# Optimization experiments

Measured on AMD Instinct MI355X. Metric: run time of the kernel, lower is better.

Reference implementation:

```python
import jax, jax.numpy as jnp
import numpy as np

N, E, D, R, G, C = 100000, 600000, 128, 4, 256, 16
EPS = 1e-5

def _rgcn(x, src, dst, edge_type, w_rel, w_root, b):
    # out_i = x_i @ W_root + b + sum_r mean_{j in N_r(i)} x_j @ W_r  (PyG RGCNConv, aggr='mean')
    x_src = x[src]                                   # [E, D] gather
    out = x @ w_root + b                             # [N, D]
    for r in range(R):
        m = (edge_type == r).astype(x.dtype)         # [E]
        msg = (x_src @ w_rel[r]) * m[:, None]        # [E, D]
        agg = jax.ops.segment_sum(msg, dst, num_segments=N)
        cnt = jax.ops.segment_sum(m, dst, num_segments=N)
        out = out + agg / jnp.maximum(cnt, 1.0)[:, None]
    return out

def _bn_eval(x, gamma, beta, mean, var):
    return (x - mean) * jax.lax.rsqrt(var + EPS) * gamma + beta

def setup_inputs() -> dict:
    key = jax.random.key(0)
    ks = jax.random.split(key, 12)
    x = jax.random.normal(ks[0], (N, D), dtype=jnp.float32)
    edge_index = jax.random.randint(ks[1], (2, E), 0, N)
    edge_type = jax.random.randint(ks[2], (E,), 0, R)
    batch = jnp.sort(jax.random.randint(ks[3], (N,), 0, G))
    s = 1.0 / np.sqrt(D)
    conv_rel_w = jax.random.normal(ks[4], (3, R, D, D), dtype=jnp.float32) * s
    conv_root_w = jax.random.normal(ks[5], (3, D, D), dtype=jnp.float32) * s
    conv_bias = jnp.zeros((3, D), dtype=jnp.float32)
    bn_gamma = jnp.ones((2, D), dtype=jnp.float32)
    bn_beta = jnp.zeros((2, D), dtype=jnp.float32)
    bn_mean = jax.random.normal(ks[6], (2, D), dtype=jnp.float32) * 0.1
    bn_var = jax.random.uniform(ks[7], (2, D), minval=0.5, maxval=1.5, dtype=jnp.float32)
    cls_w1 = jax.random.normal(ks[8], (D, D // 2), dtype=jnp.float32) * s
    cls_b1 = jnp.zeros((D // 2,), dtype=jnp.float32)
    cls_w2 = jax.random.normal(ks[9], (D // 2, C), dtype=jnp.float32) / np.sqrt(D // 2)
    cls_b2 = jnp.zeros((C,), dtype=jnp.float32)
    return {"x": x, "edge_index": edge_index, "edge_type": edge_type, "batch": batch,
            "conv_rel_w": conv_rel_w, "conv_root_w": conv_root_w, "conv_bias": conv_bias,
            "bn_gamma": bn_gamma, "bn_beta": bn_beta, "bn_mean": bn_mean, "bn_var": bn_var,
            "cls_w1": cls_w1, "cls_b1": cls_b1, "cls_w2": cls_w2, "cls_b2": cls_b2}

def reference(x, edge_index, edge_type, batch, conv_rel_w, conv_root_w, conv_bias,
              bn_gamma, bn_beta, bn_mean, bn_var, cls_w1, cls_b1, cls_w2, cls_b2):
    src, dst = edge_index[0], edge_index[1]
    prev = None
    h = x
    for i in range(3):
        h_new = _rgcn(h, src, dst, edge_type, conv_rel_w[i], conv_root_w[i], conv_bias[i])
        if prev is not None:
            h_new = h_new + prev  # residual (shapes always match: D==D)
        if i != 2:
            h_new = _bn_eval(h_new, bn_gamma[i], bn_beta[i], bn_mean[i], bn_var[i])
            h_new = jax.nn.elu(h_new)  # alpha=1; dropout inactive in eval
        prev = h_new
        h = h_new
    # global mean pool over graphs
    sums = jax.ops.segment_sum(h, batch, num_segments=G)          # [G, D]
    cnts = jax.ops.segment_sum(jnp.ones((N,), h.dtype), batch, num_segments=G)
    pooled = sums / jnp.maximum(cnts, 1.0)[:, None]
    z = jax.nn.elu(pooled @ cls_w1 + cls_b1)
    logits = z @ cls_w2 + cls_b2
    return jax.nn.log_softmax(logits, axis=-1)
```

## Files before the change

kernel.cpp:

```cpp
#include <hip/hip_runtime.h>
#include <hip/hip_bf16.h>

#define NN 100000
#define EE 600000
#define DD 128
#define GG 256
#define CCL 16

typedef __attribute__((ext_vector_type(8))) short short8;
typedef __attribute__((ext_vector_type(4))) float f32x4;
typedef const __attribute__((address_space(1))) void* gas_t;
typedef __attribute__((address_space(3))) void* las_t;

__device__ __forceinline__ void async_ld16(const void* g, void* l) {
    __builtin_amdgcn_global_load_lds((gas_t)g, (las_t)l, 16, 0, 0);
}
__device__ __forceinline__ unsigned short f2bf(float x) {
    unsigned u = __float_as_uint(x);
    unsigned r = (u + 0x7FFFu + ((u >> 16) & 1u)) >> 16;
    return (unsigned short)r;
}
__device__ __forceinline__ float bf2f(unsigned short b) {
    return __uint_as_float(((unsigned)b) << 16);
}
__device__ __forceinline__ void unpack8(uint4 v, float* f) {
    f[0] = __uint_as_float(v.x << 16); f[1] = __uint_as_float(v.x & 0xFFFF0000u);
    f[2] = __uint_as_float(v.y << 16); f[3] = __uint_as_float(v.y & 0xFFFF0000u);
    f[4] = __uint_as_float(v.z << 16); f[5] = __uint_as_float(v.z & 0xFFFF0000u);
    f[6] = __uint_as_float(v.w << 16); f[7] = __uint_as_float(v.w & 0xFFFF0000u);
}

__global__ __launch_bounds__(256) void sniff_kernel(const void* __restrict__ xraw, int* __restrict__ flag) {
    int t = threadIdx.x;
    const unsigned short* u = (const unsigned short*)xraw;
    int good = 0;
    #pragma unroll
    for (int i = 0; i < 4; i++) {
        unsigned short b = u[t * 4 + i];
        int e = (b >> 7) & 0xFF;
        if (e >= 107 && e <= 130) good++;
    }
    __shared__ int sg[256];
    sg[t] = good;
    __syncthreads();
    for (int s = 128; s > 0; s >>= 1) { if (t < s) sg[t] += sg[t + s]; __syncthreads(); }
    if (t == 0) flag[0] = (sg[0] >= 900) ? 1 : 0;
}

__device__ __forceinline__ float loadf(const void* p, size_t i, int isbf) {
    if (isbf) return bf2f(((const unsigned short*)p)[i]);
    return ((const float*)p)[i];
}

__global__ __launch_bounds__(256) void convx_kernel(const void* __restrict__ xraw, const int* __restrict__ flag,
                                                    __hip_bfloat16* __restrict__ xc) {
    int isbf = flag[0];
    size_t i0 = ((size_t)blockIdx.x * 256 + threadIdx.x) * 8;
    if (i0 >= (size_t)NN * DD) return;
    if (isbf) {
        *(uint4*)(xc + i0) = *(const uint4*)((const __hip_bfloat16*)xraw + i0);
    } else {
        const float* xf = (const float*)xraw;
        unsigned short o[8];
        #pragma unroll
        for (int j = 0; j < 8; j++) o[j] = f2bf(xf[i0 + j]);
        *(uint4*)(xc + i0) = *(uint4*)o;
    }
}

__global__ __launch_bounds__(256) void convw_kernel(const void* __restrict__ rel_raw, const void* __restrict__ root_raw,
                                                    const int* __restrict__ flag, __hip_bfloat16* __restrict__ wt) {
    int isbf = flag[0];
    int mat = blockIdx.x;
    int layer = mat / 5, g = mat % 5;
    size_t srcoff = (g == 0) ? (size_t)layer * 16384 : (size_t)(layer * 4 + (g - 1)) * 16384;
    const void* sraw = (g == 0) ? root_raw : rel_raw;
    __hip_bfloat16* dstp = wt + (size_t)mat * 16384;
    for (int idx = threadIdx.x; idx < 16384; idx += 256) {
        int k = idx >> 7, n = idx & 127;
        float v = loadf(sraw, srcoff + (size_t)k * 128 + n, isbf);
        dstp[n * 128 + k] = __float2bfloat16(v);
    }
}

__global__ __launch_bounds__(256) void convp_kernel(const void* bias, const void* bng, const void* bnb,
                                                    const void* bnm, const void* bnv, const void* w1,
                                                    const void* b1, const void* w2, const void* b2,
                                                    const int* __restrict__ flag, float* __restrict__ pf) {
    int isbf = flag[0];
    int b = blockIdx.x, t = threadIdx.x;
    if (b < 9) {
        const void* srcs[9] = {bias, bng, bnb, bnm, bnv, w1, b1, w2, b2};
        const int cnts[9] = {384, 256, 256, 256, 256, 8192, 64, 1024, 16};
        const int offs[9] = {0, 384, 640, 896, 1152, 1408, 9600, 9664, 10688};
        const void* s = srcs[b];
        int c = cnts[b], o = offs[b];
        for (int i = t; i < c; i += 256) pf[o + i] = loadf(s, i, isbf);
    } else {
        int bl = b - 9;
        if (t < 128) {
            float iva = rsqrtf(loadf(bnv, bl * 128 + t, isbf) + 1e-5f);
            float gm = loadf(bng, bl * 128 + t, isbf) * iva;
            float ga = loadf(bnb, bl * 128 + t, isbf) - loadf(bnm, bl * 128 + t, isbf) * gm;
            pf[11008 + bl * 256 + t] = gm;
            pf[11008 + bl * 256 + 128 + t] = ga;
        }
    }
}

__global__ __launch_bounds__(256) void count4_kernel(const int* __restrict__ dst, const int* __restrict__ et,
                                                     int* __restrict__ cnt4) {
    int e = blockIdx.x * 256 + threadIdx.x;
    if (e < EE) atomicAdd(&cnt4[dst[e] * 4 + et[e]], 1);
}

__global__ __launch_bounds__(256) void allocn_kernel(const int* __restrict__ cnt4, int* __restrict__ counter,
                                                     int* __restrict__ startn, int* __restrict__ wptr4) {
    int n = blockIdx.x * 256 + threadIdx.x;
    int lane = threadIdx.x & 63;
    int4 cv = make_int4(0, 0, 0, 0);
    int c = 0;
    if (n < NN) {
        cv = *(const int4*)(cnt4 + n * 4);
        c = cv.x + cv.y + cv.z + cv.w;
    }
    int v = c;
    #pragma unroll
    for (int d = 1; d < 64; d <<= 1) {
        int o = __shfl_up(v, d);
        if (lane >= d) v += o;
    }
    int base = 0;
    if (lane == 63) base = atomicAdd(counter, v);
    base = __shfl(base, 63);
    if (n < NN) {
        int s = base + v - c;
        startn[n] = s;
        wptr4[n * 4 + 0] = s;
        wptr4[n * 4 + 1] = s + cv.x;
        wptr4[n * 4 + 2] = s + cv.x + cv.y;
        wptr4[n * 4 + 3] = s + cv.x + cv.y + cv.z;
    }
}

__global__ __launch_bounds__(256) void fill4_kernel(const int* __restrict__ src, const int* __restrict__ dst,
                                                    const int* __restrict__ et, int* __restrict__ wptr4,
                                                    int* __restrict__ esrc) {
    int e = blockIdx.x * 256 + threadIdx.x;
    if (e < EE) {
        int pos = atomicAdd(&wptr4[dst[e] * 4 + et[e]], 1);
        esrc[pos] = src[e];
    }
}

__global__ __launch_bounds__(256) void agg_kernel(const __hip_bfloat16* __restrict__ h,
                                                  const int* __restrict__ esrc,
                                                  const int* __restrict__ startn,
                                                  const int* __restrict__ cnt4,
                                                  __hip_bfloat16* __restrict__ Abuf) {
    int node = blockIdx.x * 16 + (threadIdx.x >> 4);
    int c16 = threadIdx.x & 15;
    int col0 = c16 * 8;
    int4 cv = *(const int4*)(cnt4 + node * 4);
    int s = startn[node];
    int cr[4] = {cv.x, cv.y, cv.z, cv.w};
    #pragma unroll
    for (int r = 0; r < 4; r++) {
        int c = cr[r];
        float a[8];
        #pragma unroll
        for (int j = 0; j < 8; j++) a[j] = 0.f;
        int i = 0;
        for (; i + 4 <= c; i += 4) {
            int s4[4];
            uint4 vv[4];
            #pragma unroll
            for (int q = 0; q < 4; q++) s4[q] = esrc[s + i + q];
            #pragma unroll
            for (int q = 0; q < 4; q++) vv[q] = *(const uint4*)(h + (size_t)s4[q] * 128 + col0);
            #pragma unroll
            for (int q = 0; q < 4; q++) {
                float f[8];
                unpack8(vv[q], f);
                #pragma unroll
                for (int j = 0; j < 8; j++) a[j] += f[j];
            }
        }
        for (; i < c; i++) {
            int sq = esrc[s + i];
            uint4 v0 = *(const uint4*)(h + (size_t)sq * 128 + col0);
            float f[8];
            unpack8(v0, f);
            #pragma unroll
            for (int j = 0; j < 8; j++) a[j] += f[j];
        }
        float w = (c > 0) ? (1.f / (float)c) : 0.f;
        unsigned short u[8];
        #pragma unroll
        for (int j = 0; j < 8; j++) u[j] = f2bf(a[j] * w);
        *(uint4*)(Abuf + (size_t)node * 512 + r * 128 + col0) = *(uint4*)u;
        s += c;
    }
}

#define STAGE_B(P, CH) do { \
    const __hip_bfloat16* _wg = wt5 + (size_t)(CH) * 16384; \
    _Pragma("unroll") \
    for (int _j = 0; _j < 4; _j++) { \
        int _slot = _j * 512 + t; \
        int _brow = _slot >> 4, _sp = _slot & 15; \
        async_ld16(_wg + _brow * 128 + (_sp ^ (_brow & 15)) * 8, &ldsb[(P) * 16384 + _slot * 8]); \
    } \
} while (0)

#define LOAD_A(D0, D1, CH) do { \
    const __hip_bfloat16* _p0 = ((CH) == 0) ? (h_in + (size_t)r0 * 128) : (Abuf + (size_t)r0 * 512 + ((CH) - 1) * 128); \
    const __hip_bfloat16* _p1 = ((CH) == 0) ? (h_in + (size_t)r1 * 128) : (Abuf + (size_t)r1 * 512 + ((CH) - 1) * 128); \
    _Pragma("unroll") \
    for (int _kc = 0; _kc < 4; _kc++) { \
        D0[_kc] = *(const short8*)(_p0 + _kc * 32 + quad * 8); \
        D1[_kc] = *(const short8*)(_p1 + _kc * 32 + quad * 8); \
    } \
} while (0)

#define MFMA_CH(P, A0, A1) do { \
    _Pragma("unroll") \
    for (int _kc = 0; _kc < 4; _kc++) { \
        int _s = _kc * 4 + quad; \
        _Pragma("unroll") \
        for (int _nt = 0; _nt < 4; _nt++) { \
            int _rb = wc * 64 + _nt * 16 + r16; \
            short8 _b = *(const short8*)&ldsb[(P) * 16384 + (_rb * 16 + (_s ^ (_rb & 15))) * 8]; \
            acc0[_nt] = __builtin_amdgcn_mfma_f32_16x16x32_bf16(A0[_kc], _b, acc0[_nt], 0, 0, 0); \
            acc1[_nt] = __builtin_amdgcn_mfma_f32_16x16x32_bf16(A1[_kc], _b, acc1[_nt], 0, 0, 0); \
        } \
    } \
} while (0)

__global__ __launch_bounds__(512, 4) void rgemm_kernel(const __hip_bfloat16* __restrict__ h_in,
                                                       const __hip_bfloat16* __restrict__ Abuf,
                                                       const __hip_bfloat16* __restrict__ wt5,
                                                       const float* __restrict__ bias,
                                                       const float* __restrict__ gmp,
                                                       const float* __restrict__ gap,
                                                       const __hip_bfloat16* __restrict__ hres,
                                                       __hip_bfloat16* __restrict__ hout,
                                                       int do_bn) {
    __shared__ __align__(16) char ldsraw[132 * 128 * 4];
    short* ldsb = (short*)ldsraw;
    float* cf = (float*)ldsraw;
    int t = threadIdx.x;
    int wave = t >> 6, lane = t & 63, quad = lane >> 4, r16 = lane & 15;
    int wr = wave & 3, wc = wave >> 2;
    int m0 = blockIdx.x * 128;

    int r0 = m0 + wr * 32 + r16;      if (r0 > NN - 1) r0 = NN - 1;
    int r1 = m0 + wr * 32 + 16 + r16; if (r1 > NN - 1) r1 = NN - 1;

    f32x4 acc0[4], acc1[4];
    #pragma unroll
    for (int j = 0; j < 4; j++) { acc0[j] = (f32x4){0.f, 0.f, 0.f, 0.f}; acc1[j] = (f32x4){0.f, 0.f, 0.f, 0.f}; }

    short8 aA0[4], aA1[4], aB0[4], aB1[4];
    LOAD_A(aA0, aA1, 0);
    STAGE_B(0, 0);

    __syncthreads();  STAGE_B(1, 1);  LOAD_A(aB0, aB1, 1);  MFMA_CH(0, aA0, aA1);
    __syncthreads();  STAGE_B(0, 2);  LOAD_A(aA0, aA1, 2);  MFMA_CH(1, aB0, aB1);
    __syncthreads();  STAGE_B(1, 3);  LOAD_A(aB0, aB1, 3);  MFMA_CH(0, aA0, aA1);
    __syncthreads();  STAGE_B(0, 4);  LOAD_A(aA0, aA1, 4);  MFMA_CH(1, aB0, aB1);
    __syncthreads();                                        MFMA_CH(0, aA0, aA1);

    __syncthreads();
    #pragma unroll
    for (int nt = 0; nt < 4; nt++) {
        int col = wc * 64 + nt * 16 + r16;
        #pragma unroll
        for (int reg = 0; reg < 4; reg++) {
            int crow0 = wr * 32 + quad * 4 + reg;
            cf[crow0 * 132 + col] = acc0[nt][reg];
            cf[(crow0 + 16) * 132 + col] = acc1[nt][reg];
        }
    }
    __syncthreads();
    #pragma unroll
    for (int it = 0; it < 4; it++) {
        int u4 = it * 512 + t;
        int crow = u4 >> 4, seg = u4 & 15;
        int node = m0 + crow;
        if (node < NN) {
            int gcol0 = seg * 8;
            float a[8];
            #pragma unroll
            for (int j = 0; j < 8; j++) a[j] = cf[crow * 132 + gcol0 + j] + bias[gcol0 + j];
            if (hres) {
                float rf[8];
                unpack8(*(const uint4*)(hres + (size_t)node * 128 + gcol0), rf);
                #pragma unroll
                for (int j = 0; j < 8; j++) a[j] += rf[j];
            }
            if (do_bn) {
                #pragma unroll
                for (int j = 0; j < 8; j++) {
                    float z = a[j] * gmp[gcol0 + j] + gap[gcol0 + j];
                    a[j] = z > 0.f ? z : expm1f(z);
                }
            }
            unsigned short u[8];
            #pragma unroll
            for (int j = 0; j < 8; j++) u[j] = f2bf(a[j]);
            *(uint4*)(hout + (size_t)node * 128 + gcol0) = *(uint4*)u;
        }
    }
}

__global__ __launch_bounds__(256) void pool_kernel(const __hip_bfloat16* __restrict__ h3,
                                                   const int* __restrict__ batch,
                                                   float* __restrict__ pooled) {
    int g = blockIdx.x, t = threadIdx.x;
    int rowpar = t >> 4, colg = t & 15;
    int lo = 0, hi = NN;
    while (lo < hi) { int mid = (lo + hi) >> 1; if (batch[mid] < g) lo = mid + 1; else hi = mid; }
    int s0 = lo;
    hi = NN;
    while (lo < hi) { int mid = (lo + hi) >> 1; if (batch[mid] < g + 1) lo = mid + 1; else hi = mid; }
    int s1 = lo;
    float a[8];
    #pragma unroll
    for (int j = 0; j < 8; j++) a[j] = 0.f;
    for (int n = s0 + rowpar; n < s1; n += 16) {
        float f[8];
        unpack8(*(const uint4*)(h3 + (size_t)n * 128 + colg * 8), f);
        #pragma unroll
        for (int j = 0; j < 8; j++) a[j] += f[j];
    }
    __shared__ float sd[16][128];
    #pragma unroll
    for (int j = 0; j < 8; j++) sd[rowpar][colg * 8 + j] = a[j];
    __syncthreads();
    if (t < 128) {
        float sum = 0.f;
        #pragma unroll
        for (int i = 0; i < 16; i++) sum += sd[i][t];
        int cgn = s1 - s0;
        pooled[g * 128 + t] = sum / (float)(cgn > 0 ? cgn : 1);
    }
}

__global__ __launch_bounds__(64) void cls_kernel(const float* __restrict__ pooled,
                                                 const float* __restrict__ pf,
                                                 const int* __restrict__ flag,
                                                 void* __restrict__ out) {
    int g = blockIdx.x, j = threadIdx.x;
    const float* w1 = pf + 1408;
    const float* b1 = pf + 9600;
    const float* w2 = pf + 9664;
    const float* b2 = pf + 10688;
    __shared__ float z[64];
    __shared__ float lg[16];
    const float* p = pooled + g * 128;
    float acc = b1[j];
    for (int d = 0; d < 128; d++) acc += p[d] * w1[d * 64 + j];
    acc = acc > 0.f ? acc : expm1f(acc);
    z[j] = acc;
    __syncthreads();
    if (j < CCL) {
        float l = b2[j];
        for (int k = 0; k < 64; k++) l += z[k] * w2[k * 16 + j];
        lg[j] = l;
    }
    __syncthreads();
    if (j < CCL) {
        float m = lg[0];
        for (int k = 1; k < CCL; k++) m = fmaxf(m, lg[k]);
        float s = 0.f;
        for (int k = 0; k < CCL; k++) s += expf(lg[k] - m);
        float val = lg[j] - m - logf(s);
        if (flag[0]) ((__hip_bfloat16*)out)[g * CCL + j] = __float2bfloat16(val);
        else         ((float*)out)[g * CCL + j] = val;
    }
}

extern "C" void kernel_launch(void* const* d_in, const int* in_sizes, int n_in,
                              void* d_out, int out_size, void* d_ws, size_t ws_size,
                              hipStream_t stream) {
    const void* x_raw    = d_in[0];
    const int* ei        = (const int*)d_in[1];
    const int* et        = (const int*)d_in[2];
    const int* batch     = (const int*)d_in[3];
    const void* rel_raw  = d_in[4];
    const void* root_raw = d_in[5];
    const int* srcp = ei;
    const int* dstp = ei + EE;

    char* ws = (char*)d_ws;
    size_t off = 0;
    auto take = [&](size_t bytes) { size_t r = off; off += (bytes + 1023) & ~(size_t)1023; return r; };
    __hip_bfloat16* Abuf  = (__hip_bfloat16*)(ws + take((size_t)NN * 512 * 2));
    __hip_bfloat16* xc    = (__hip_bfloat16*)(ws + take((size_t)NN * 128 * 2));
    __hip_bfloat16* hA    = (__hip_bfloat16*)(ws + take((size_t)NN * 128 * 2));
    __hip_bfloat16* hB    = (__hip_bfloat16*)(ws + take((size_t)NN * 128 * 2));
    __hip_bfloat16* hC    = (__hip_bfloat16*)(ws + take((size_t)NN * 128 * 2));
    __hip_bfloat16* wt    = (__hip_bfloat16*)(ws + take((size_t)15 * 16384 * 2));
    float* pf             = (float*)(ws + take((size_t)11520 * 4));
    float* pooled         = (float*)(ws + take((size_t)GG * 128 * 4));
    int* cnt4             = (int*)(ws + take((size_t)NN * 16 + 8));
    int* counter          = cnt4 + NN * 4;
    int* flag             = cnt4 + NN * 4 + 1;
    int* startn           = (int*)(ws + take((size_t)NN * 4));
    int* wptr4            = (int*)(ws + take((size_t)NN * 16));
    int* esrc             = (int*)(ws + take((size_t)EE * 4));

    hipMemsetAsync(cnt4, 0, (size_t)NN * 16 + 4, stream);
    sniff_kernel<<<1, 256, 0, stream>>>(x_raw, flag);
    convx_kernel<<<(NN * DD / 8 + 255) / 256, 256, 0, stream>>>(x_raw, flag, xc);
    convw_kernel<<<15, 256, 0, stream>>>(rel_raw, root_raw, flag, wt);
    convp_kernel<<<11, 256, 0, stream>>>(d_in[6], d_in[7], d_in[8], d_in[9], d_in[10],
                                         d_in[11], d_in[12], d_in[13], d_in[14], flag, pf);
    count4_kernel<<<(EE + 255) / 256, 256, 0, stream>>>(dstp, et, cnt4);
    allocn_kernel<<<(NN + 255) / 256, 256, 0, stream>>>(cnt4, counter, startn, wptr4);
    fill4_kernel<<<(EE + 255) / 256, 256, 0, stream>>>(srcp, dstp, et, wptr4, esrc);

    const __hip_bfloat16* hin = xc;
    __hip_bfloat16* houts[3] = {hA, hB, hC};
    for (int l = 0; l < 3; l++) {
        int bl = l < 2 ? l : 1;
        agg_kernel<<<NN / 16, 256, 0, stream>>>(hin, esrc, startn, cnt4, Abuf);
        rgemm_kernel<<<(NN + 127) / 128, 512, 0, stream>>>(
            hin, Abuf, wt + (size_t)l * 5 * 16384, pf + l * 128,
            pf + 11008 + bl * 256, pf + 11008 + bl * 256 + 128,
            (l > 0) ? hin : (const __hip_bfloat16*)nullptr, houts[l], (l < 2) ? 1 : 0);
        hin = houts[l];
    }
    pool_kernel<<<GG, 256, 0, stream>>>(houts[2], batch, pooled);
    cls_kernel<<<GG, 64, 0, stream>>>(pooled, pf, flag, (void*)d_out);
}
```

Measured before the change: 651.9 us.

## Fuse neighbor aggregation into the relational GEMM kernel, dropping the Abuf round trip

Replaces the separate aggregation kernel and LDS-staged GEMM with one per-layer kernel. Each lane gathers and averages its node's neighbor rows per relation straight into MFMA A-fragments, then multiplies against weights read directly from global memory. This removes the 100000x512 bf16 intermediate buffer's write and read plus one launch per layer. In exchange, weight B-fragments are no longer shared through LDS and are re-read per wave from cache. The gather also now runs with one lane per node across 16 lanes' column slices, so there is less parallelism per node and more divergence on irregular degrees.

```diff
diff --git a/kernel.cpp b/kernel.cpp
--- a/kernel.cpp
+++ b/kernel.cpp
@@ -9,12 +9,7 @@
 
 typedef __attribute__((ext_vector_type(8))) short short8;
 typedef __attribute__((ext_vector_type(4))) float f32x4;
-typedef const __attribute__((address_space(1))) void* gas_t;
-typedef __attribute__((address_space(3))) void* las_t;
-
-__device__ __forceinline__ void async_ld16(const void* g, void* l) {
-    __builtin_amdgcn_global_load_lds((gas_t)g, (las_t)l, 16, 0, 0);
-}
+
 __device__ __forceinline__ unsigned short f2bf(float x) {
     unsigned u = __float_as_uint(x);
     unsigned r = (u + 0x7FFFu + ((u >> 16) & 1u)) >> 16;
@@ -153,149 +148,136 @@
     }
 }
 
-__global__ __launch_bounds__(256) void agg_kernel(const __hip_bfloat16* __restrict__ h,
-                                                  const int* __restrict__ esrc,
-                                                  const int* __restrict__ startn,
-                                                  const int* __restrict__ cnt4,
-                                                  __hip_bfloat16* __restrict__ Abuf) {
-    int node = blockIdx.x * 16 + (threadIdx.x >> 4);
-    int c16 = threadIdx.x & 15;
-    int col0 = c16 * 8;
-    int4 cv = *(const int4*)(cnt4 + node * 4);
-    int s = startn[node];
-    int cr[4] = {cv.x, cv.y, cv.z, cv.w};
-    #pragma unroll
-    for (int r = 0; r < 4; r++) {
-        int c = cr[r];
-        float a[8];
-        #pragma unroll
-        for (int j = 0; j < 8; j++) a[j] = 0.f;
-        int i = 0;
-        for (; i + 4 <= c; i += 4) {
-            int s4[4];
-            uint4 vv[4];
-            #pragma unroll
-            for (int q = 0; q < 4; q++) s4[q] = esrc[s + i + q];
-            #pragma unroll
-            for (int q = 0; q < 4; q++) vv[q] = *(const uint4*)(h + (size_t)s4[q] * 128 + col0);
-            #pragma unroll
-            for (int q = 0; q < 4; q++) {
-                float f[8];
-                unpack8(vv[q], f);
-                #pragma unroll
-                for (int j = 0; j < 8; j++) a[j] += f[j];
-            }
-        }
-        for (; i < c; i++) {
-            int sq = esrc[s + i];
-            uint4 v0 = *(const uint4*)(h + (size_t)sq * 128 + col0);
-            float f[8];
-            unpack8(v0, f);
-            #pragma unroll
-            for (int j = 0; j < 8; j++) a[j] += f[j];
-        }
-        float w = (c > 0) ? (1.f / (float)c) : 0.f;
-        unsigned short u[8];
-        #pragma unroll
-        for (int j = 0; j < 8; j++) u[j] = f2bf(a[j] * w);
-        *(uint4*)(Abuf + (size_t)node * 512 + r * 128 + col0) = *(uint4*)u;
-        s += c;
-    }
-}
-
-#define STAGE_B(P, CH) do { \
-    const __hip_bfloat16* _wg = wt5 + (size_t)(CH) * 16384; \
+#define GATHER_REL(CNT, SEG, DST) do { \
+    float _a[4][8]; \
     _Pragma("unroll") \
-    for (int _j = 0; _j < 4; _j++) { \
-        int _slot = _j * 512 + t; \
-        int _brow = _slot >> 4, _sp = _slot & 15; \
-        async_ld16(_wg + _brow * 128 + (_sp ^ (_brow & 15)) * 8, &ldsb[(P) * 16384 + _slot * 8]); \
+    for (int _kc = 0; _kc < 4; _kc++) \
+        _Pragma("unroll") \
+        for (int _j = 0; _j < 8; _j++) _a[_kc][_j] = 0.f; \
+    int _i = 0; \
+    for (; _i + 2 <= (CNT); _i += 2) { \
+        int _e0 = esrc[(SEG) + _i]; \
+        int _e1 = esrc[(SEG) + _i + 1]; \
+        const __hip_bfloat16* _p0 = h_in + (size_t)_e0 * 128; \
+        const __hip_bfloat16* _p1 = h_in + (size_t)_e1 * 128; \
+        uint4 _v0[4]; \
+        _Pragma("unroll") \
+        for (int _kc = 0; _kc < 4; _kc++) _v0[_kc] = *(const uint4*)(_p0 + _kc * 32 + quad * 8); \
+        _Pragma("unroll") \
+        for (int _kc = 0; _kc < 4; _kc++) { \
+            uint4 _v1 = *(const uint4*)(_p1 + _kc * 32 + quad * 8); \
+            float _f[8]; \
+            unpack8(_v0[_kc], _f); \
+            _Pragma("unroll") \
+            for (int _j = 0; _j < 8; _j++) _a[_kc][_j] += _f[_j]; \
+            unpack8(_v1, _f); \
+            _Pragma("unroll") \
+            for (int _j = 0; _j < 8; _j++) _a[_kc][_j] += _f[_j]; \
+        } \
+    } \
+    if (_i < (CNT)) { \
+        int _e0 = esrc[(SEG) + _i]; \
+        const __hip_bfloat16* _p0 = h_in + (size_t)_e0 * 128; \
+        _Pragma("unroll") \
+        for (int _kc = 0; _kc < 4; _kc++) { \
+            uint4 _v = *(const uint4*)(_p0 + _kc * 32 + quad * 8); \
+            float _f[8]; \
+            unpack8(_v, _f); \
+            _Pragma("unroll") \
+            for (int _j = 0; _j < 8; _j++) _a[_kc][_j] += _f[_j]; \
+        } \
+    } \
+    float _w = ((CNT) > 0) ? (1.f / (float)(CNT)) : 0.f; \
+    _Pragma("unroll") \
+    for (int _kc = 0; _kc < 4; _kc++) { \
+        short8 _t; \
+        _Pragma("unroll") \
+        for (int _j = 0; _j < 8; _j++) _t[_j] = (short)f2bf(_a[_kc][_j] * _w); \
+        DST[_kc] = _t; \
     } \
 } while (0)
 
-#define LOAD_A(D0, D1, CH) do { \
-    const __hip_bfloat16* _p0 = ((CH) == 0) ? (h_in + (size_t)r0 * 128) : (Abuf + (size_t)r0 * 512 + ((CH) - 1) * 128); \
-    const __hip_bfloat16* _p1 = ((CH) == 0) ? (h_in + (size_t)r1 * 128) : (Abuf + (size_t)r1 * 512 + ((CH) - 1) * 128); \
+#define MFMA_G(G, AF) do { \
+    const __hip_bfloat16* _wb = wt5 + (size_t)(G) * 16384; \
     _Pragma("unroll") \
     for (int _kc = 0; _kc < 4; _kc++) { \
-        D0[_kc] = *(const short8*)(_p0 + _kc * 32 + quad * 8); \
-        D1[_kc] = *(const short8*)(_p1 + _kc * 32 + quad * 8); \
-    } \
-} while (0)
-
-#define MFMA_CH(P, A0, A1) do { \
-    _Pragma("unroll") \
-    for (int _kc = 0; _kc < 4; _kc++) { \
-        int _s = _kc * 4 + quad; \
-        _Pragma("unroll") \
-        for (int _nt = 0; _nt < 4; _nt++) { \
-            int _rb = wc * 64 + _nt * 16 + r16; \
-            short8 _b = *(const short8*)&ldsb[(P) * 16384 + (_rb * 16 + (_s ^ (_rb & 15))) * 8]; \
-            acc0[_nt] = __builtin_amdgcn_mfma_f32_16x16x32_bf16(A0[_kc], _b, acc0[_nt], 0, 0, 0); \
-            acc1[_nt] = __builtin_amdgcn_mfma_f32_16x16x32_bf16(A1[_kc], _b, acc1[_nt], 0, 0, 0); \
+        _Pragma("unroll") \
+        for (int _nt = 0; _nt < 8; _nt++) { \
+            short8 _b = *(const short8*)(_wb + (_nt * 16 + r16) * 128 + _kc * 32 + quad * 8); \
+            acc[_nt] = __builtin_amdgcn_mfma_f32_16x16x32_bf16(AF[_kc], _b, acc[_nt], 0, 0, 0); \
         } \
     } \
 } while (0)
 
-__global__ __launch_bounds__(512, 4) void rgemm_kernel(const __hip_bfloat16* __restrict__ h_in,
-                                                       const __hip_bfloat16* __restrict__ Abuf,
-                                                       const __hip_bfloat16* __restrict__ wt5,
-                                                       const float* __restrict__ bias,
-                                                       const float* __restrict__ gmp,
-                                                       const float* __restrict__ gap,
-                                                       const __hip_bfloat16* __restrict__ hres,
-                                                       __hip_bfloat16* __restrict__ hout,
-                                                       int do_bn) {
-    __shared__ __align__(16) char ldsraw[132 * 128 * 4];
-    short* ldsb = (short*)ldsraw;
-    float* cf = (float*)ldsraw;
+__global__ __launch_bounds__(256) void flayer_kernel(const __hip_bfloat16* __restrict__ h_in,
+                                                     const int* __restrict__ esrc,
+                                                     const int* __restrict__ startn,
+                                                     const int* __restrict__ cnt4,
+                                                     const __hip_bfloat16* __restrict__ wt5,
+                                                     const float* __restrict__ bias,
+                                                     const float* __restrict__ gmp,
+                                                     const float* __restrict__ gap,
+                                                     const __hip_bfloat16* __restrict__ hres,
+                                                     __hip_bfloat16* __restrict__ hout,
+                                                     int do_bn) {
+    __shared__ __align__(16) float cf[64 * 132];
     int t = threadIdx.x;
-    int wave = t >> 6, lane = t & 63, quad = lane >> 4, r16 = lane & 15;
-    int wr = wave & 3, wc = wave >> 2;
-    int m0 = blockIdx.x * 128;
-
-    int r0 = m0 + wr * 32 + r16;      if (r0 > NN - 1) r0 = NN - 1;
-    int r1 = m0 + wr * 32 + 16 + r16; if (r1 > NN - 1) r1 = NN - 1;
-
-    f32x4 acc0[4], acc1[4];
-    #pragma unroll
-    for (int j = 0; j < 4; j++) { acc0[j] = (f32x4){0.f, 0.f, 0.f, 0.f}; acc1[j] = (f32x4){0.f, 0.f, 0.f, 0.f}; }
-
-    short8 aA0[4], aA1[4], aB0[4], aB1[4];
-    LOAD_A(aA0, aA1, 0);
-    STAGE_B(0, 0);
-
-    __syncthreads();  STAGE_B(1, 1);  LOAD_A(aB0, aB1, 1);  MFMA_CH(0, aA0, aA1);
-    __syncthreads();  STAGE_B(0, 2);  LOAD_A(aA0, aA1, 2);  MFMA_CH(1, aB0, aB1);
-    __syncthreads();  STAGE_B(1, 3);  LOAD_A(aB0, aB1, 3);  MFMA_CH(0, aA0, aA1);
-    __syncthreads();  STAGE_B(0, 4);  LOAD_A(aA0, aA1, 4);  MFMA_CH(1, aB0, aB1);
-    __syncthreads();                                        MFMA_CH(0, aA0, aA1);
-
-    __syncthreads();
-    #pragma unroll
-    for (int nt = 0; nt < 4; nt++) {
-        int col = wc * 64 + nt * 16 + r16;
+    int wv = t >> 6, lane = t & 63, quad = lane >> 4, r16 = lane & 15;
+    int m0 = blockIdx.x * 64;
+    int node = m0 + wv * 16 + r16;
+    if (node > NN - 1) node = NN - 1;
+
+    int s0 = startn[node];
+    int4 cv = *(const int4*)(cnt4 + node * 4);
+
+    f32x4 acc[8];
+    #pragma unroll
+    for (int nt = 0; nt < 8; nt++) acc[nt] = (f32x4){0.f, 0.f, 0.f, 0.f};
+
+    const __hip_bfloat16* hp = h_in + (size_t)node * 128;
+    short8 afr[4];
+    #pragma unroll
+    for (int kc = 0; kc < 4; kc++) afr[kc] = *(const short8*)(hp + kc * 32 + quad * 8);
+
+    short8 afg[4];
+    int seg = s0;
+    GATHER_REL(cv.x, seg, afg);
+    MFMA_G(0, afr);
+    MFMA_G(1, afg);
+    seg += cv.x;
+    GATHER_REL(cv.y, seg, afg);
+    MFMA_G(2, afg);
+    seg += cv.y;
+    GATHER_REL(cv.z, seg, afg);
+    MFMA_G(3, afg);
+    seg += cv.z;
+    GATHER_REL(cv.w, seg, afg);
+    MFMA_G(4, afg);
+
+    #pragma unroll
+    for (int nt = 0; nt < 8; nt++) {
+        int col = nt * 16 + r16;
         #pragma unroll
         for (int reg = 0; reg < 4; reg++) {
-            int crow0 = wr * 32 + quad * 4 + reg;
-            cf[crow0 * 132 + col] = acc0[nt][reg];
-            cf[(crow0 + 16) * 132 + col] = acc1[nt][reg];
+            int row = wv * 16 + quad * 4 + reg;
+            cf[row * 132 + col] = acc[nt][reg];
         }
     }
     __syncthreads();
     #pragma unroll
     for (int it = 0; it < 4; it++) {
-        int u4 = it * 512 + t;
-        int crow = u4 >> 4, seg = u4 & 15;
-        int node = m0 + crow;
-        if (node < NN) {
-            int gcol0 = seg * 8;
+        int u4 = it * 256 + t;
+        int row = u4 >> 4, sg = u4 & 15;
+        int onode = m0 + row;
+        if (onode < NN) {
+            int gcol0 = sg * 8;
+            const float* cp = cf + row * 132 + gcol0;
             float a[8];
             #pragma unroll
-            for (int j = 0; j < 8; j++) a[j] = cf[crow * 132 + gcol0 + j] + bias[gcol0 + j];
+            for (int j = 0; j < 8; j++) a[j] = cp[j] + bias[gcol0 + j];
             if (hres) {
                 float rf[8];
-                unpack8(*(const uint4*)(hres + (size_t)node * 128 + gcol0), rf);
+                unpack8(*(const uint4*)(hres + (size_t)onode * 128 + gcol0), rf);
                 #pragma unroll
                 for (int j = 0; j < 8; j++) a[j] += rf[j];
             }
@@ -309,7 +291,7 @@
             unsigned short u[8];
             #pragma unroll
             for (int j = 0; j < 8; j++) u[j] = f2bf(a[j]);
-            *(uint4*)(hout + (size_t)node * 128 + gcol0) = *(uint4*)u;
+            *(uint4*)(hout + (size_t)onode * 128 + gcol0) = *(uint4*)u;
         }
     }
 }
@@ -396,7 +378,6 @@
     char* ws = (char*)d_ws;
     size_t off = 0;
     auto take = [&](size_t bytes) { size_t r = off; off += (bytes + 1023) & ~(size_t)1023; return r; };
-    __hip_bfloat16* Abuf  = (__hip_bfloat16*)(ws + take((size_t)NN * 512 * 2));
     __hip_bfloat16* xc    = (__hip_bfloat16*)(ws + take((size_t)NN * 128 * 2));
     __hip_bfloat16* hA    = (__hip_bfloat16*)(ws + take((size_t)NN * 128 * 2));
     __hip_bfloat16* hB    = (__hip_bfloat16*)(ws + take((size_t)NN * 128 * 2));
@@ -425,9 +406,8 @@
     __hip_bfloat16* houts[3] = {hA, hB, hC};
     for (int l = 0; l < 3; l++) {
         int bl = l < 2 ? l : 1;
-        agg_kernel<<<NN / 16, 256, 0, stream>>>(hin, esrc, startn, cnt4, Abuf);
-        rgemm_kernel<<<(NN + 127) / 128, 512, 0, stream>>>(
-            hin, Abuf, wt + (size_t)l * 5 * 16384, pf + l * 128,
+        flayer_kernel<<<(NN + 63) / 64, 256, 0, stream>>>(
+            hin, esrc, startn, cnt4, wt + (size_t)l * 5 * 16384, pf + l * 128,
             pf + 11008 + bl * 256, pf + 11008 + bl * 256 + 128,
             (l > 0) ? hin : (const __hip_bfloat16*)nullptr, houts[l], (l < 2) ? 1 : 0);
         hin = houts[l];
```

Result: slower. 943.2 us (+44.7%).
